# Kernel tuning notes

Measured on AMD Instinct MI355X. Metric: run time of the kernel, lower is better.

## Reference

```python
import jax, jax.numpy as jnp
import numpy as np

N = 50000      # nodes
E = 800000     # edges (before self-loops)
B = 50         # graphs in batch
F_IN = 16      # node features
HID = 64       # hidden_dim (= per-head channels, concat=False)
H = 4          # heads
ED = 5         # edge_dim
OUT = 3        # output_dim


def setup_inputs() -> dict:
    key = jax.random.key(0)
    ks = jax.random.split(key, 32)
    g = lambda k, shape, s=0.1: jax.random.normal(k, shape, dtype=jnp.float32) * s
    x = jax.random.normal(ks[0], (N, F_IN), dtype=jnp.float32)
    edge_index = jax.random.randint(ks[1], (2, E), 0, N)
    edge_attr = jax.random.normal(ks[2], (E, ED), dtype=jnp.float32)
    batch = jnp.repeat(jnp.arange(B), N // B)  # sorted segment ids, each graph non-empty
    inp = dict(
        x=x, edge_index=edge_index, edge_attr=edge_attr, batch=batch,
        # edge_encoder: Linear(5,64) -> ReLU -> Linear(64,1) -> Sigmoid
        ee_w1=g(ks[3], (ED, HID)), ee_b1=jnp.zeros((HID,), jnp.float32),
        ee_w2=g(ks[4], (HID, 1)), ee_b2=jnp.zeros((1,), jnp.float32),
        # GATConv params (PyG, edge_dim=1 semantics for the scalar edge weight)
        W1=g(ks[5], (F_IN, H * HID)),              # conv1 lin (bias=False)
        Ws=g(ks[6], (2, HID, H * HID)),            # convs[0..1] lin
        att_src=g(ks[7], (3, H, HID)),
        att_dst=g(ks[8], (3, H, HID)),
        We=g(ks[9], (3, 1, H * HID)),              # lin_edge (bias=False)
        att_e=g(ks[10], (3, H, HID)),
        bias=jnp.zeros((3, HID), jnp.float32),     # conv bias (concat=False -> [HID])
        ln_g=jnp.ones((HID,), jnp.float32), ln_b=jnp.zeros((HID,), jnp.float32),
        lin1_w=g(ks[11], (HID, HID)), lin1_b=jnp.zeros((HID,), jnp.float32),
        lin2_w=g(ks[12], (HID, OUT)), lin2_b=jnp.zeros((OUT,), jnp.float32),
    )
    return inp


def _gat_conv(xin, src, dst, ew, W, a_s, a_d, W_e, a_e, b):
    # xin: [N, Fin]; src/dst: [Et]; ew: [Et] per-edge scalar weight
    h = (xin @ W).reshape(N, H, HID)                      # [N,H,C]
    alpha_src = (h * a_s).sum(-1)                         # [N,H]
    alpha_dst = (h * a_d).sum(-1)                         # [N,H]
    he = (ew[:, None] * W_e.reshape(1, H * HID)).reshape(-1, H, HID)  # lin_edge
    alpha_e = (he * a_e).sum(-1)                          # [Et,H]
    alpha = jax.nn.leaky_relu(alpha_src[src] + alpha_dst[dst] + alpha_e, 0.2)
    # segment softmax over destination nodes
    m = jax.ops.segment_max(alpha, dst, num_segments=N)   # [N,H]
    p = jnp.exp(alpha - m[dst])
    s = jax.ops.segment_sum(p, dst, num_segments=N)
    a = p / (s[dst] + 1e-16)                              # [Et,H]
    out = jax.ops.segment_sum(h[src] * a[:, :, None], dst, num_segments=N)  # [N,H,C]
    return out.mean(axis=1) + b                           # concat=False -> mean heads


def reference(x, edge_index, edge_attr, batch, ee_w1, ee_b1, ee_w2, ee_b2,
              W1, Ws, att_src, att_dst, We, att_e, bias,
              ln_g, ln_b, lin1_w, lin1_b, lin2_w, lin2_b):
    # edge-attribute MLP -> per-edge scalar weight in (0,1)
    ew = jax.nn.sigmoid(jax.nn.relu(edge_attr @ ee_w1 + ee_b1) @ ee_w2 + ee_b2).reshape(-1)
    # add self-loops (PyG default, fill_value='mean' for edge weight)
    loops = jnp.arange(N)
    src = jnp.concatenate([edge_index[0], loops])
    dst = jnp.concatenate([edge_index[1], loops])
    ew = jnp.concatenate([ew, jnp.full((N,), ew.mean(), dtype=ew.dtype)])

    xi = jax.nn.elu(_gat_conv(x, src, dst, ew, W1, att_src[0], att_dst[0], We[0], att_e[0], bias[0]))
    for l in range(2):  # residual layers (dropout is identity in eval)
        xn = _gat_conv(xi, src, dst, ew, Ws[l], att_src[l + 1], att_dst[l + 1], We[l + 1], att_e[l + 1], bias[l + 1])
        xi = jax.nn.elu(xi + xn)

    mu = xi.mean(-1, keepdims=True)
    var = ((xi - mu) ** 2).mean(-1, keepdims=True)
    xln = (xi - mu) / jnp.sqrt(var + 1e-5) * ln_g + ln_b

    targets = jnp.searchsorted(batch, jnp.arange(B))      # first node of each graph
    t = jax.nn.elu(xln[targets] @ lin1_w + lin1_b)
    return t @ lin2_w + lin2_b                            # [B, 3]
```

## Files before the change

kernel.cpp:

```cpp
#include <hip/hip_runtime.h>
#include <cstddef>
#include <cstdint>

constexpr int NN = 50000;
constexpr int NE = 800000;
constexpr int ET = NE + NN;
constexpr int NB = 50;
constexpr int SCAN_B = 1024;
constexpr int NBLK = (NN + SCAN_B - 1) / SCAN_B;
constexpr int NPB_F = 16;
constexpr int NPB_T = 8;
constexpr int NTB_F = NN / NPB_F;
constexpr int MLPB = (ET + 1023) / 1024;

typedef float v2f __attribute__((ext_vector_type(2)));

__device__ __forceinline__ float eluf(float x) { return x > 0.f ? x : expm1f(x); }

__device__ __forceinline__ unsigned short f2bf(float f) {
    unsigned int u = __float_as_uint(f);
    unsigned int r = (u + 0x7fffu + ((u >> 16) & 1u)) >> 16;
    return (unsigned short)r;
}

template <int NPB, typename NodeOf>
__device__ __forceinline__ void alpha_reduce_store(const float* acc, float as_t, float ad_t,
                                                   int lane, int head, NodeOf nodeOf,
                                                   float* __restrict__ asrc,
                                                   float* __restrict__ adst) {
    #pragma unroll
    for (int g = 0; g < NPB; g += 4) {
        float x0, x1, x2, x3;
        {
            float vs, vd;
            vs = acc[g + 0] * as_t; vd = acc[g + 0] * ad_t;
            x0 = ((lane & 1) ? vd : vs) + __shfl_xor((lane & 1) ? vs : vd, 1);
            vs = acc[g + 1] * as_t; vd = acc[g + 1] * ad_t;
            x1 = ((lane & 1) ? vd : vs) + __shfl_xor((lane & 1) ? vs : vd, 1);
            vs = acc[g + 2] * as_t; vd = acc[g + 2] * ad_t;
            x2 = ((lane & 1) ? vd : vs) + __shfl_xor((lane & 1) ? vs : vd, 1);
            vs = acc[g + 3] * as_t; vd = acc[g + 3] * ad_t;
            x3 = ((lane & 1) ? vd : vs) + __shfl_xor((lane & 1) ? vs : vd, 1);
        }
        float y0 = ((lane & 2) ? x1 : x0) + __shfl_xor((lane & 2) ? x0 : x1, 2);
        float y1 = ((lane & 2) ? x3 : x2) + __shfl_xor((lane & 2) ? x2 : x3, 2);
        float z  = ((lane & 4) ? y1 : y0) + __shfl_xor((lane & 4) ? y0 : y1, 4);
        z += __shfl_xor(z, 8);
        z += __shfl_xor(z, 16);
        z += __shfl_xor(z, 32);
        if (lane < 8) {
            int node = nodeOf(g + (lane >> 1));
            if (lane & 1) adst[node * 4 + head] = z;
            else          asrc[node * 4 + head] = z;
        }
    }
}

__device__ __forceinline__ void aggregate_one_node(
        int widx, int lane,
        const unsigned short* __restrict__ hb,
        const float* __restrict__ asrc, const float* __restrict__ adst,
        const int2* __restrict__ csr, const float* __restrict__ ce_l,
        const float* __restrict__ bias_l, const int* __restrict__ row_ptr,
        float* __restrict__ xi, int residual) {
    int half = lane >> 5;
    int li = lane & 31;
    int head = li >> 3;
    int start = row_ptr[widx], end = row_ptr[widx + 1];
    float adw = adst[widx * 4 + head];
    float ceh = ce_l[head];
    const uint4* hbv = (const uint4*)hb;

    v2f acc2[4];
    #pragma unroll
    for (int r = 0; r < 4; ++r) { acc2[r].x = 0.f; acc2[r].y = 0.f; }
    float psum = 0.f;

    #define PROC(EI)                                                                  \
        {                                                                             \
            const int2 se = csr[EI];                                                  \
            int s = se.x;                                                             \
            float w = __int_as_float(se.y);                                           \
            const uint4 q = hbv[(unsigned)s * 32u + (unsigned)li];                    \
            float v = asrc[s * 4 + head] + adw + w * ceh;                             \
            v = v > 0.f ? v : 0.2f * v;                                               \
            float p = __expf(v);                                                      \
            psum += p;                                                                \
            v2f pv; pv.x = p; pv.y = p;                                               \
            v2f h0; h0.x = __uint_as_float(q.x << 16); h0.y = __uint_as_float(q.x & 0xffff0000u); \
            v2f h1; h1.x = __uint_as_float(q.y << 16); h1.y = __uint_as_float(q.y & 0xffff0000u); \
            v2f h2; h2.x = __uint_as_float(q.z << 16); h2.y = __uint_as_float(q.z & 0xffff0000u); \
            v2f h3; h3.x = __uint_as_float(q.w << 16); h3.y = __uint_as_float(q.w & 0xffff0000u); \
            acc2[0] += pv * h0;                                                       \
            acc2[1] += pv * h1;                                                       \
            acc2[2] += pv * h2;                                                       \
            acc2[3] += pv * h3;                                                       \
        }

    int ei = start + half;
    for (; ei + 2 < end; ei += 4) {
        PROC(ei);
        PROC(ei + 2);
    }
    if (ei < end) PROC(ei);
    #undef PROC

    float acc[8];
    acc[0] = acc2[0].x; acc[1] = acc2[0].y; acc[2] = acc2[1].x; acc[3] = acc2[1].y;
    acc[4] = acc2[2].x; acc[5] = acc2[2].y; acc[6] = acc2[3].x; acc[7] = acc2[3].y;

    psum += __shfl_xor(psum, 32);
    #pragma unroll
    for (int r = 0; r < 8; ++r) acc[r] += __shfl_xor(acc[r], 32);

    float inv = 1.f / (psum + 1e-16f);
    #pragma unroll
    for (int r = 0; r < 8; ++r) acc[r] *= inv;

    #pragma unroll
    for (int r = 0; r < 8; ++r) {
        acc[r] += __shfl_xor(acc[r], 8);
        acc[r] += __shfl_xor(acc[r], 16);
        acc[r] *= 0.25f;
    }

    if (lane < 8) {
        int c0 = lane * 8;
        const float4 b0 = *(const float4*)(bias_l + c0);
        const float4 b1 = *(const float4*)(bias_l + c0 + 4);
        float4 v0, v1;
        v0.x = acc[0] + b0.x; v0.y = acc[1] + b0.y; v0.z = acc[2] + b0.z; v0.w = acc[3] + b0.w;
        v1.x = acc[4] + b1.x; v1.y = acc[5] + b1.y; v1.z = acc[6] + b1.z; v1.w = acc[7] + b1.w;
        float* xo = xi + (size_t)widx * 64 + c0;
        if (residual) {
            const float4 p0 = *(const float4*)xo;
            const float4 p1 = *(const float4*)(xo + 4);
            v0.x += p0.x; v0.y += p0.y; v0.z += p0.z; v0.w += p0.w;
            v1.x += p1.x; v1.y += p1.y; v1.z += p1.z; v1.w += p1.w;
        }
        v0.x = eluf(v0.x); v0.y = eluf(v0.y); v0.z = eluf(v0.z); v0.w = eluf(v0.w);
        v1.x = eluf(v1.x); v1.y = eluf(v1.y); v1.z = eluf(v1.z); v1.w = eluf(v1.w);
        *(float4*)xo = v0;
        *(float4*)(xo + 4) = v1;
    }
}

__global__ void front_kernel(const float* __restrict__ xin, const float* __restrict__ W,
                             const float* __restrict__ a_s, const float* __restrict__ a_d,
                             unsigned short* __restrict__ hb, float* __restrict__ asrc,
                             float* __restrict__ adst,
                             const float* __restrict__ ea,
                             const float* __restrict__ w1, const float* __restrict__ b1,
                             const float* __restrict__ w2, const float* __restrict__ b2,
                             const int* __restrict__ ei_dst, int* __restrict__ deg,
                             int2* __restrict__ ewp, float* __restrict__ ew_sum) {
    __shared__ float wt[64 * 8];
    __shared__ float wsum[4];
    __shared__ unsigned short hs[NPB_F * 256];
    const int t = threadIdx.x;
    if (blockIdx.x < NTB_F) {
        const int FIN = 16;
        const int n0 = blockIdx.x * NPB_F;
        float acc[NPB_F];
        #pragma unroll
        for (int i = 0; i < NPB_F; ++i) acc[i] = 0.f;
        #pragma unroll 4
        for (int k = 0; k < FIN; ++k) {
            float wv = W[k * 256 + t];
            #pragma unroll
            for (int i = 0; i < NPB_F; ++i)
                acc[i] += xin[(size_t)(n0 + i) * FIN + k] * wv;
        }
        int lane = t & 63, head = t >> 6;
        #pragma unroll
        for (int i = 0; i < NPB_F; ++i) hs[i * 256 + t] = f2bf(acc[i]);
        alpha_reduce_store<NPB_F>(acc, a_s[t], a_d[t], lane, head,
                                  [&](int i) { return n0 + i; }, asrc, adst);
        __syncthreads();
        ((uint4*)(hb + (size_t)n0 * 256))[t]       = ((const uint4*)hs)[t];
        ((uint4*)(hb + (size_t)n0 * 256))[t + 256] = ((const uint4*)hs)[t + 256];
    } else {
        if (t < 64) {
            #pragma unroll
            for (int i = 0; i < 5; ++i) wt[t * 8 + i] = w1[i * 64 + t];
            wt[t * 8 + 5] = b1[t];
            wt[t * 8 + 6] = w2[t];
            wt[t * 8 + 7] = 0.f;
        }
        __syncthreads();
        const int e0 = (blockIdx.x - NTB_F) * 1024 + t;
        float a0[4], a1[4], a2[4], a3[4], a4[4], acc[4];
        #pragma unroll
        for (int m = 0; m < 4; ++m) {
            int e = e0 + 256 * m;
            if (e < NE) {
                a0[m] = ea[e*5+0]; a1[m] = ea[e*5+1]; a2[m] = ea[e*5+2];
                a3[m] = ea[e*5+3]; a4[m] = ea[e*5+4];
            } else {
                a0[m] = a1[m] = a2[m] = a3[m] = a4[m] = 0.f;
            }
            acc[m] = b2[0];
        }
        int pos[4] = {0, 0, 0, 0};
        #pragma unroll
        for (int m = 0; m < 4; ++m) {
            int e = e0 + 256 * m;
            if (e < ET) {
                int d = (e < NE) ? ei_dst[e] : (e - NE);
                pos[m] = atomicAdd(&deg[d], 1);
            }
        }
        #pragma unroll 4
        for (int j = 0; j < 64; ++j) {
            const float4 lo = *(const float4*)&wt[j * 8];
            const float4 hi = *(const float4*)&wt[j * 8 + 4];
            #pragma unroll
            for (int m = 0; m < 4; ++m) {
                float hj = hi.y + a0[m]*lo.x + a1[m]*lo.y + a2[m]*lo.z + a3[m]*lo.w + a4[m]*hi.x;
                acc[m] += fmaxf(hj, 0.f) * hi.z;
            }
        }
        float vsum = 0.f;
        #pragma unroll
        for (int m = 0; m < 4; ++m) {
            int e = e0 + 256 * m;
            if (e < NE) {
                float val = 1.f / (1.f + __expf(-acc[m]));
                ewp[e] = make_int2(pos[m], __float_as_int(val));
                vsum += val;
            } else if (e < ET) {
                ewp[e] = make_int2(pos[m], 0);
            }
        }
        #pragma unroll
        for (int m = 1; m <= 32; m <<= 1) vsum += __shfl_xor(vsum, m);
        if ((t & 63) == 0) wsum[t >> 6] = vsum;
        __syncthreads();
        if (t == 0) atomicAdd(ew_sum, (wsum[0] + wsum[1]) + (wsum[2] + wsum[3]));
    }
}

__global__ void scan_blocks(const int* __restrict__ deg, int* __restrict__ row_ptr,
                            int* __restrict__ bsum,
                            const float* __restrict__ We, const float* __restrict__ att_e,
                            float* __restrict__ ce) {
    __shared__ int sdata[SCAN_B];
    int t = threadIdx.x;
    int i = blockIdx.x * SCAN_B + t;
    if (i < 12) {
        int l = i >> 2, h = i & 3;
        float s = 0.f;
        for (int c = 0; c < 64; ++c)
            s += We[l*256 + h*64 + c] * att_e[l*256 + h*64 + c];
        ce[i] = s;
    }
    int v = (i < NN) ? deg[i] : 0;
    sdata[t] = v;
    __syncthreads();
    for (int off = 1; off < SCAN_B; off <<= 1) {
        int tv = (t >= off) ? sdata[t - off] : 0;
        __syncthreads();
        sdata[t] += tv;
        __syncthreads();
    }
    if (i < NN) row_ptr[i + 1] = sdata[t];
    if (t == SCAN_B - 1) bsum[blockIdx.x] = sdata[t];
}

__global__ void scan_fixup(const int* __restrict__ bsum, int* __restrict__ row_ptr) {
    __shared__ int sboff[64];
    int t = threadIdx.x;
    if (t < 64) {
        int v = (t < NBLK) ? bsum[t] : 0;
        int inc = v;
        #pragma unroll
        for (int off = 1; off < 64; off <<= 1) {
            int n = __shfl_up(inc, off);
            if (t >= off) inc += n;
        }
        sboff[t] = inc - v;
    }
    __syncthreads();
    int i = blockIdx.x * 256 + t;
    if (i < NN) row_ptr[i + 1] += sboff[i >> 10];
    if (i == 0) row_ptr[0] = 0;
}

__global__ void scatter_kernel(const int* __restrict__ ei_src, const int* __restrict__ ei_dst,
                               const int* __restrict__ row_ptr, const int2* __restrict__ ewp,
                               const float* __restrict__ ew_sum, int2* __restrict__ csr) {
    int e = blockIdx.x * 256 + threadIdx.x;
    if (e >= ET) return;
    int2 pw = ewp[e];
    int d, s, wbits;
    if (e < NE) {
        d = ei_dst[e];
        s = ei_src[e];
        wbits = pw.y;
    } else {
        d = s = e - NE;
        wbits = __float_as_int(ew_sum[0] * (1.f / (float)NE));
    }
    csr[row_ptr[d] + pw.x] = make_int2(s, wbits);
}

__global__ void mark1_kernel(const int* __restrict__ batch, const int* __restrict__ row_ptr,
                             const int2* __restrict__ csr, int* __restrict__ flag1,
                             int* __restrict__ list1, int* __restrict__ cnt1,
                             int* __restrict__ tgt) {
    int b = blockIdx.x;
    int t = threadIdx.x;
    __shared__ int tg_s;
    if (t == 0) {
        int lo = 0, hi = NN;
        while (lo < hi) {
            int mid = (lo + hi) >> 1;
            if (batch[mid] < b) lo = mid + 1; else hi = mid;
        }
        tg_s = lo;
        tgt[b] = lo;
    }
    __syncthreads();
    int tg = tg_s;
    int start = row_ptr[tg], end = row_ptr[tg + 1];
    for (int j = start + t; j < end; j += 64) {
        int s = csr[j].x;
        if (atomicExch(&flag1[s], 1) == 0) {
            int p = atomicAdd(cnt1, 1);
            if (p < NN) list1[p] = s;
        }
    }
}

__global__ void mark2_kernel(const int* __restrict__ row_ptr, const int2* __restrict__ csr,
                             const int* __restrict__ list1, const int* __restrict__ cnt1,
                             int* __restrict__ flag2, int* __restrict__ list2,
                             int* __restrict__ cnt2) {
    int i = blockIdx.x * 256 + threadIdx.x;
    if (i >= cnt1[0] || i >= NN) return;
    int u = list1[i];
    int start = row_ptr[u], end = row_ptr[u + 1];
    for (int j = start; j < end; ++j) {
        int s = csr[j].x;
        if (atomicExch(&flag2[s], 1) == 0) {
            int p = atomicAdd(cnt2, 1);
            if (p < NN) list2[p] = s;
        }
    }
}

__global__ void transform64_list(const int* __restrict__ list, const int* __restrict__ cnt,
                                 const float* __restrict__ xin, const float* __restrict__ W,
                                 const float* __restrict__ a_s, const float* __restrict__ a_d,
                                 unsigned short* __restrict__ hb, float* __restrict__ asrc,
                                 float* __restrict__ adst) {
    const int t = threadIdx.x;
    const int n0 = blockIdx.x * NPB_T;
    const int nv = min(cnt[0], NN);
    if (n0 >= nv) return;
    __shared__ unsigned short hs[NPB_T * 256];
    __shared__ int nls[NPB_T];
    if (t < NPB_T) nls[t] = list[min(n0 + t, nv - 1)];
    __syncthreads();
    int nreg[NPB_T];
    #pragma unroll
    for (int i = 0; i < NPB_T; ++i) nreg[i] = nls[i];
    float acc[NPB_T];
    #pragma unroll
    for (int i = 0; i < NPB_T; ++i) acc[i] = 0.f;
    #pragma unroll 4
    for (int k = 0; k < 64; ++k) {
        float wv = W[k * 256 + t];
        #pragma unroll
        for (int i = 0; i < NPB_T; ++i)
            acc[i] += xin[(size_t)nreg[i] * 64 + k] * wv;
    }
    int lane = t & 63, head = t >> 6;
    #pragma unroll
    for (int i = 0; i < NPB_T; ++i) hs[i * 256 + t] = f2bf(acc[i]);
    alpha_reduce_store<NPB_T>(acc, a_s[t], a_d[t], lane, head,
                              [&](int i) { return nls[i]; }, asrc, adst);
    __syncthreads();
    int nn = nls[t >> 5];
    ((uint4*)(hb + (size_t)nn * 256))[t & 31] = ((const uint4*)hs)[t];
}

__global__ void gat_aggregate_list(const int* __restrict__ list, const int* __restrict__ cnt,
                                   int cnt_const,
                                   const unsigned short* __restrict__ hb,
                                   const float* __restrict__ asrc, const float* __restrict__ adst,
                                   const int2* __restrict__ csr, const float* __restrict__ ce_l,
                                   const float* __restrict__ bias_l,
                                   const int* __restrict__ row_ptr,
                                   float* __restrict__ xi, int residual) {
    int idx = (blockIdx.x * 256 + threadIdx.x) >> 6;
    int n = cnt ? min(cnt[0], NN) : cnt_const;
    if (idx >= n) return;
    int widx = list[idx];
    int lane = threadIdx.x & 63;
    aggregate_one_node(widx, lane, hb, asrc, adst, csr, ce_l, bias_l, row_ptr, xi, residual);
}

__global__ void readout_kernel(const float* __restrict__ xi, const int* __restrict__ tgt,
                               const float* __restrict__ ln_g, const float* __restrict__ ln_b,
                               const float* __restrict__ l1w, const float* __restrict__ l1b,
                               const float* __restrict__ l2w, const float* __restrict__ l2b,
                               float* __restrict__ out) {
    int b = blockIdx.x;
    int t = threadIdx.x;
    int tg = tgt[b];
    float x = xi[(size_t)tg * 64 + t];
    float s = x;
    #pragma unroll
    for (int mask = 1; mask <= 32; mask <<= 1) s += __shfl_xor(s, mask);
    float mu = s * (1.f / 64.f);
    float d = x - mu;
    float v = d * d;
    #pragma unroll
    for (int mask = 1; mask <= 32; mask <<= 1) v += __shfl_xor(v, mask);
    float var = v * (1.f / 64.f);
    float xn = d * rsqrtf(var + 1e-5f) * ln_g[t] + ln_b[t];
    __shared__ float sx[64];
    sx[t] = xn;
    __syncthreads();
    float acc = l1b[t];
    for (int k = 0; k < 64; ++k) acc += sx[k] * l1w[k * 64 + t];
    acc = eluf(acc);
    __shared__ float st[64];
    st[t] = acc;
    __syncthreads();
    if (t < 3) {
        float o = l2b[t];
        for (int k = 0; k < 64; ++k) o += st[k] * l2w[k * 3 + t];
        out[b * 3 + t] = o;
    }
}

extern "C" void kernel_launch(void* const* d_in, const int* in_sizes, int n_in,
                              void* d_out, int out_size, void* d_ws, size_t ws_size,
                              hipStream_t stream) {
    const float* x        = (const float*)d_in[0];
    const int*   ei       = (const int*)d_in[1];
    const float* ea       = (const float*)d_in[2];
    const int*   batch    = (const int*)d_in[3];
    const float* ee_w1    = (const float*)d_in[4];
    const float* ee_b1    = (const float*)d_in[5];
    const float* ee_w2    = (const float*)d_in[6];
    const float* ee_b2    = (const float*)d_in[7];
    const float* W1       = (const float*)d_in[8];
    const float* Ws       = (const float*)d_in[9];
    const float* att_src  = (const float*)d_in[10];
    const float* att_dst  = (const float*)d_in[11];
    const float* We       = (const float*)d_in[12];
    const float* att_e    = (const float*)d_in[13];
    const float* bias     = (const float*)d_in[14];
    const float* ln_g     = (const float*)d_in[15];
    const float* ln_b     = (const float*)d_in[16];
    const float* lin1_w   = (const float*)d_in[17];
    const float* lin1_b   = (const float*)d_in[18];
    const float* lin2_w   = (const float*)d_in[19];
    const float* lin2_b   = (const float*)d_in[20];
    float* out = (float*)d_out;

    char* ws = (char*)d_ws;
    size_t off = 0;
    auto alloc = [&](size_t bytes) -> char* {
        char* p = ws + off;
        off += (bytes + 255) & ~(size_t)255;
        return p;
    };
    int2*  ewp     = (int2*)alloc((size_t)ET * 8);
    float* ce      = (float*)alloc(12 * 4);
    unsigned short* hbuf = (unsigned short*)alloc((size_t)NN * 256 * 2);
    float* asrc    = (float*)alloc((size_t)NN * 4 * 4);
    float* adst    = (float*)alloc((size_t)NN * 4 * 4);
    float* xi      = (float*)alloc((size_t)NN * 64 * 4);
    int*   deg     = (int*)alloc(((size_t)NN * 3 + 64) * 4);
    int*   flag1   = deg + NN;
    int*   flag2   = deg + 2 * NN;
    float* ew_sum  = (float*)(deg + 3 * NN);
    int*   cnt1    = deg + 3 * NN + 1;
    int*   cnt2    = deg + 3 * NN + 2;
    int*   row_ptr = (int*)alloc((size_t)(NN + 1) * 4);
    int*   bsum    = (int*)alloc(64 * 4);
    int2*  csr     = (int2*)alloc((size_t)ET * 8);
    int*   list1   = (int*)alloc((size_t)NN * 4);
    int*   list2   = (int*)alloc((size_t)NN * 4);
    int*   tgt     = (int*)alloc(NB * 4);
    (void)ws_size; (void)n_in; (void)in_sizes; (void)out_size;

    const int* ei_src = ei;
    const int* ei_dst = ei + NE;

    hipMemsetAsync(deg, 0, ((size_t)NN * 3 + 64) * 4, stream);
    front_kernel<<<NTB_F + MLPB, 256, 0, stream>>>(x, W1, att_src + 0 * 256, att_dst + 0 * 256,
                                                   hbuf, asrc, adst,
                                                   ea, ee_w1, ee_b1, ee_w2, ee_b2,
                                                   ei_dst, deg, ewp, ew_sum);

    scan_blocks<<<NBLK, SCAN_B, 0, stream>>>(deg, row_ptr, bsum, We, att_e, ce);
    scan_fixup<<<(NN + 255) / 256, 256, 0, stream>>>(bsum, row_ptr);
    scatter_kernel<<<(ET + 255) / 256, 256, 0, stream>>>(ei_src, ei_dst, row_ptr, ewp, ew_sum, csr);

    mark1_kernel<<<NB, 64, 0, stream>>>(batch, row_ptr, csr, flag1, list1, cnt1, tgt);
    mark2_kernel<<<(NN + 255) / 256, 256, 0, stream>>>(row_ptr, csr, list1, cnt1,
                                                       flag2, list2, cnt2);

    gat_aggregate_list<<<(NN + 3) / 4, 256, 0, stream>>>(list2, cnt2, 0, hbuf, asrc, adst,
                                                         csr, ce + 0 * 4, bias + 0 * 64,
                                                         row_ptr, xi, 0);
    transform64_list<<<NN / NPB_T, 256, 0, stream>>>(list2, cnt2, xi, Ws + 0 * 64 * 256,
                                                     att_src + 1 * 256, att_dst + 1 * 256,
                                                     hbuf, asrc, adst);
    gat_aggregate_list<<<(NN + 3) / 4, 256, 0, stream>>>(list1, cnt1, 0, hbuf, asrc, adst,
                                                         csr, ce + 1 * 4, bias + 1 * 64,
                                                         row_ptr, xi, 1);
    transform64_list<<<NN / NPB_T, 256, 0, stream>>>(list1, cnt1, xi, Ws + 1 * 64 * 256,
                                                     att_src + 2 * 256, att_dst + 2 * 256,
                                                     hbuf, asrc, adst);
    gat_aggregate_list<<<(NB + 3) / 4, 256, 0, stream>>>(tgt, nullptr, NB, hbuf, asrc, adst,
                                                         csr, ce + 2 * 4, bias + 2 * 64,
                                                         row_ptr, xi, 1);

    readout_kernel<<<NB, 64, 0, stream>>>(xi, tgt, ln_g, ln_b, lin1_w, lin1_b, lin2_w, lin2_b, out);
}
```

Measured before the change: 301.6 us.

## Mark receptive-field nodes from raw edges and scatter only needed CSR rows

Computes the 1-hop and 2-hop target neighbourhood flags directly from the raw edge list, folded into the front and scan kernels as extra blocks, instead of separate mark kernels that walk the CSR. The scatter kernel then writes CSR entries only for destinations in the 2-hop set, which cuts scatter writes. The last-layer aggregation is fused with the readout, removing two launches. The cost is extra full edge passes with atomics inside front and scan, and the ordering now relies on flag1 being complete before the scan kernel's marking blocks run.

```diff
diff --git a/kernel.cpp b/kernel.cpp
--- a/kernel.cpp
+++ b/kernel.cpp
@@ -12,6 +12,8 @@
 constexpr int NPB_T = 8;
 constexpr int NTB_F = NN / NPB_F;
 constexpr int MLPB = (ET + 1023) / 1024;
+constexpr int MRKB  = (ET + 255) / 256;
+constexpr int MRK2B = (ET + 1023) / 1024;
 
 typedef float v2f __attribute__((ext_vector_type(2)));
 
@@ -56,13 +58,14 @@
     }
 }
 
+template <bool WRITE_LDS>
 __device__ __forceinline__ void aggregate_one_node(
         int widx, int lane,
         const unsigned short* __restrict__ hb,
         const float* __restrict__ asrc, const float* __restrict__ adst,
         const int2* __restrict__ csr, const float* __restrict__ ce_l,
         const float* __restrict__ bias_l, const int* __restrict__ row_ptr,
-        float* __restrict__ xi, int residual) {
+        float* __restrict__ xi, int residual, float* xs_row) {
     int half = lane >> 5;
     int li = lane & 31;
     int head = li >> 3;
@@ -142,6 +145,10 @@
         v1.x = eluf(v1.x); v1.y = eluf(v1.y); v1.z = eluf(v1.z); v1.w = eluf(v1.w);
         *(float4*)xo = v0;
         *(float4*)(xo + 4) = v1;
+        if (WRITE_LDS) {
+            *(float4*)(xs_row + c0) = v0;
+            *(float4*)(xs_row + c0 + 4) = v1;
+        }
     }
 }
 
@@ -152,8 +159,11 @@
                              const float* __restrict__ ea,
                              const float* __restrict__ w1, const float* __restrict__ b1,
                              const float* __restrict__ w2, const float* __restrict__ b2,
-                             const int* __restrict__ ei_dst, int* __restrict__ deg,
-                             int2* __restrict__ ewp, float* __restrict__ ew_sum) {
+                             const int* __restrict__ ei_src, const int* __restrict__ ei_dst,
+                             int* __restrict__ deg,
+                             int2* __restrict__ ewp, float* __restrict__ ew_sum,
+                             const int* __restrict__ batch, int* __restrict__ flag1,
+                             int* __restrict__ list1, int* __restrict__ cnt1) {
     __shared__ float wt[64 * 8];
     __shared__ float wsum[4];
     __shared__ unsigned short hs[NPB_F * 256];
@@ -179,7 +189,7 @@
         __syncthreads();
         ((uint4*)(hb + (size_t)n0 * 256))[t]       = ((const uint4*)hs)[t];
         ((uint4*)(hb + (size_t)n0 * 256))[t + 256] = ((const uint4*)hs)[t + 256];
-    } else {
+    } else if (blockIdx.x < NTB_F + MLPB) {
         if (t < 64) {
             #pragma unroll
             for (int i = 0; i < 5; ++i) wt[t * 8 + i] = w1[i * 64 + t];
@@ -237,15 +247,41 @@
         if ((t & 63) == 0) wsum[t >> 6] = vsum;
         __syncthreads();
         if (t == 0) atomicAdd(ew_sum, (wsum[0] + wsum[1]) + (wsum[2] + wsum[3]));
+    } else {
+        int e = (blockIdx.x - NTB_F - MLPB) * 256 + t;
+        if (e < ET) {
+            int d, s;
+            if (e < NE) { d = ei_dst[e]; s = ei_src[e]; } else { d = s = e - NE; }
+            bool is_t = (d == 0) || (batch[d] != batch[d - 1]);
+            if (is_t && atomicExch(&flag1[s], 1) == 0) {
+                int p = atomicAdd(cnt1, 1);
+                if (p < NN) list1[p] = s;
+            }
+        }
     }
 }
 
 __global__ void scan_blocks(const int* __restrict__ deg, int* __restrict__ row_ptr,
                             int* __restrict__ bsum,
                             const float* __restrict__ We, const float* __restrict__ att_e,
-                            float* __restrict__ ce) {
+                            float* __restrict__ ce,
+                            const int* __restrict__ ei_src, const int* __restrict__ ei_dst,
+                            const int* __restrict__ flag1, int* __restrict__ flag2,
+                            int* __restrict__ list2, int* __restrict__ cnt2) {
     __shared__ int sdata[SCAN_B];
     int t = threadIdx.x;
+    if (blockIdx.x >= NBLK) {
+        int e = (blockIdx.x - NBLK) * 1024 + t;
+        if (e < ET) {
+            int d, s;
+            if (e < NE) { d = ei_dst[e]; s = ei_src[e]; } else { d = s = e - NE; }
+            if (flag1[d] && atomicExch(&flag2[s], 1) == 0) {
+                int p = atomicAdd(cnt2, 1);
+                if (p < NN) list2[p] = s;
+            }
+        }
+        return;
+    }
     int i = blockIdx.x * SCAN_B + t;
     if (i < 12) {
         int l = i >> 2, h = i & 3;
@@ -288,65 +324,22 @@
 
 __global__ void scatter_kernel(const int* __restrict__ ei_src, const int* __restrict__ ei_dst,
                                const int* __restrict__ row_ptr, const int2* __restrict__ ewp,
-                               const float* __restrict__ ew_sum, int2* __restrict__ csr) {
+                               const float* __restrict__ ew_sum, const int* __restrict__ flag2,
+                               int2* __restrict__ csr) {
     int e = blockIdx.x * 256 + threadIdx.x;
     if (e >= ET) return;
+    int d = (e < NE) ? ei_dst[e] : (e - NE);
+    if (!flag2[d]) return;
     int2 pw = ewp[e];
-    int d, s, wbits;
+    int s, wbits;
     if (e < NE) {
-        d = ei_dst[e];
         s = ei_src[e];
         wbits = pw.y;
     } else {
-        d = s = e - NE;
+        s = d;
         wbits = __float_as_int(ew_sum[0] * (1.f / (float)NE));
     }
     csr[row_ptr[d] + pw.x] = make_int2(s, wbits);
-}
-
-__global__ void mark1_kernel(const int* __restrict__ batch, const int* __restrict__ row_ptr,
-                             const int2* __restrict__ csr, int* __restrict__ flag1,
-                             int* __restrict__ list1, int* __restrict__ cnt1,
-                             int* __restrict__ tgt) {
-    int b = blockIdx.x;
-    int t = threadIdx.x;
-    __shared__ int tg_s;
-    if (t == 0) {
-        int lo = 0, hi = NN;
-        while (lo < hi) {
-            int mid = (lo + hi) >> 1;
-            if (batch[mid] < b) lo = mid + 1; else hi = mid;
-        }
-        tg_s = lo;
-        tgt[b] = lo;
-    }
-    __syncthreads();
-    int tg = tg_s;
-    int start = row_ptr[tg], end = row_ptr[tg + 1];
-    for (int j = start + t; j < end; j += 64) {
-        int s = csr[j].x;
-        if (atomicExch(&flag1[s], 1) == 0) {
-            int p = atomicAdd(cnt1, 1);
-            if (p < NN) list1[p] = s;
-        }
-    }
-}
-
-__global__ void mark2_kernel(const int* __restrict__ row_ptr, const int2* __restrict__ csr,
-                             const int* __restrict__ list1, const int* __restrict__ cnt1,
-                             int* __restrict__ flag2, int* __restrict__ list2,
-                             int* __restrict__ cnt2) {
-    int i = blockIdx.x * 256 + threadIdx.x;
-    if (i >= cnt1[0] || i >= NN) return;
-    int u = list1[i];
-    int start = row_ptr[u], end = row_ptr[u + 1];
-    for (int j = start; j < end; ++j) {
-        int s = csr[j].x;
-        if (atomicExch(&flag2[s], 1) == 0) {
-            int p = atomicAdd(cnt2, 1);
-            if (p < NN) list2[p] = s;
-        }
-    }
 }
 
 __global__ void transform64_list(const int* __restrict__ list, const int* __restrict__ cnt,
@@ -386,7 +379,6 @@
 }
 
 __global__ void gat_aggregate_list(const int* __restrict__ list, const int* __restrict__ cnt,
-                                   int cnt_const,
                                    const unsigned short* __restrict__ hb,
                                    const float* __restrict__ asrc, const float* __restrict__ adst,
                                    const int2* __restrict__ csr, const float* __restrict__ ce_l,
@@ -394,22 +386,41 @@
                                    const int* __restrict__ row_ptr,
                                    float* __restrict__ xi, int residual) {
     int idx = (blockIdx.x * 256 + threadIdx.x) >> 6;
-    int n = cnt ? min(cnt[0], NN) : cnt_const;
+    int n = min(cnt[0], NN);
     if (idx >= n) return;
     int widx = list[idx];
     int lane = threadIdx.x & 63;
-    aggregate_one_node(widx, lane, hb, asrc, adst, csr, ce_l, bias_l, row_ptr, xi, residual);
-}
-
-__global__ void readout_kernel(const float* __restrict__ xi, const int* __restrict__ tgt,
-                               const float* __restrict__ ln_g, const float* __restrict__ ln_b,
-                               const float* __restrict__ l1w, const float* __restrict__ l1b,
-                               const float* __restrict__ l2w, const float* __restrict__ l2b,
-                               float* __restrict__ out) {
+    aggregate_one_node<false>(widx, lane, hb, asrc, adst, csr, ce_l, bias_l, row_ptr,
+                              xi, residual, nullptr);
+}
+
+__global__ void readout_fused(const int* __restrict__ batch,
+                              const unsigned short* __restrict__ hb,
+                              const float* __restrict__ asrc, const float* __restrict__ adst,
+                              const int2* __restrict__ csr, const float* __restrict__ ce_l,
+                              const float* __restrict__ bias_l, const int* __restrict__ row_ptr,
+                              float* __restrict__ xi,
+                              const float* __restrict__ ln_g, const float* __restrict__ ln_b,
+                              const float* __restrict__ l1w, const float* __restrict__ l1b,
+                              const float* __restrict__ l2w, const float* __restrict__ l2b,
+                              float* __restrict__ out) {
     int b = blockIdx.x;
     int t = threadIdx.x;
-    int tg = tgt[b];
-    float x = xi[(size_t)tg * 64 + t];
+    __shared__ int tg_s;
+    __shared__ float xs[64];
+    if (t == 0) {
+        int lo = 0, hi = NN;
+        while (lo < hi) {
+            int mid = (lo + hi) >> 1;
+            if (batch[mid] < b) lo = mid + 1; else hi = mid;
+        }
+        tg_s = lo;
+    }
+    __syncthreads();
+    int tg = tg_s;
+    aggregate_one_node<true>(tg, t, hb, asrc, adst, csr, ce_l, bias_l, row_ptr, xi, 1, xs);
+    __syncthreads();
+    float x = xs[t];
     float s = x;
     #pragma unroll
     for (int mask = 1; mask <= 32; mask <<= 1) s += __shfl_xor(s, mask);
@@ -420,11 +431,11 @@
     for (int mask = 1; mask <= 32; mask <<= 1) v += __shfl_xor(v, mask);
     float var = v * (1.f / 64.f);
     float xn = d * rsqrtf(var + 1e-5f) * ln_g[t] + ln_b[t];
-    __shared__ float sx[64];
-    sx[t] = xn;
+    __syncthreads();
+    xs[t] = xn;
     __syncthreads();
     float acc = l1b[t];
-    for (int k = 0; k < 64; ++k) acc += sx[k] * l1w[k * 64 + t];
+    for (int k = 0; k < 64; ++k) acc += xs[k] * l1w[k * 64 + t];
     acc = eluf(acc);
     __shared__ float st[64];
     st[t] = acc;
@@ -486,41 +497,37 @@
     int2*  csr     = (int2*)alloc((size_t)ET * 8);
     int*   list1   = (int*)alloc((size_t)NN * 4);
     int*   list2   = (int*)alloc((size_t)NN * 4);
-    int*   tgt     = (int*)alloc(NB * 4);
     (void)ws_size; (void)n_in; (void)in_sizes; (void)out_size;
 
     const int* ei_src = ei;
     const int* ei_dst = ei + NE;
 
     hipMemsetAsync(deg, 0, ((size_t)NN * 3 + 64) * 4, stream);
-    front_kernel<<<NTB_F + MLPB, 256, 0, stream>>>(x, W1, att_src + 0 * 256, att_dst + 0 * 256,
-                                                   hbuf, asrc, adst,
-                                                   ea, ee_w1, ee_b1, ee_w2, ee_b2,
-                                                   ei_dst, deg, ewp, ew_sum);
-
-    scan_blocks<<<NBLK, SCAN_B, 0, stream>>>(deg, row_ptr, bsum, We, att_e, ce);
+    front_kernel<<<NTB_F + MLPB + MRKB, 256, 0, stream>>>(
+        x, W1, att_src + 0 * 256, att_dst + 0 * 256, hbuf, asrc, adst,
+        ea, ee_w1, ee_b1, ee_w2, ee_b2, ei_src, ei_dst, deg, ewp, ew_sum,
+        batch, flag1, list1, cnt1);
+
+    scan_blocks<<<NBLK + MRK2B, SCAN_B, 0, stream>>>(deg, row_ptr, bsum, We, att_e, ce,
+                                                     ei_src, ei_dst, flag1, flag2, list2, cnt2);
     scan_fixup<<<(NN + 255) / 256, 256, 0, stream>>>(bsum, row_ptr);
-    scatter_kernel<<<(ET + 255) / 256, 256, 0, stream>>>(ei_src, ei_dst, row_ptr, ewp, ew_sum, csr);
-
-    mark1_kernel<<<NB, 64, 0, stream>>>(batch, row_ptr, csr, flag1, list1, cnt1, tgt);
-    mark2_kernel<<<(NN + 255) / 256, 256, 0, stream>>>(row_ptr, csr, list1, cnt1,
-                                                       flag2, list2, cnt2);
-
-    gat_aggregate_list<<<(NN + 3) / 4, 256, 0, stream>>>(list2, cnt2, 0, hbuf, asrc, adst,
+    scatter_kernel<<<(ET + 255) / 256, 256, 0, stream>>>(ei_src, ei_dst, row_ptr, ewp,
+                                                         ew_sum, flag2, csr);
+
+    gat_aggregate_list<<<(NN + 3) / 4, 256, 0, stream>>>(list2, cnt2, hbuf, asrc, adst,
                                                          csr, ce + 0 * 4, bias + 0 * 64,
                                                          row_ptr, xi, 0);
     transform64_list<<<NN / NPB_T, 256, 0, stream>>>(list2, cnt2, xi, Ws + 0 * 64 * 256,
                                                      att_src + 1 * 256, att_dst + 1 * 256,
                                                      hbuf, asrc, adst);
-    gat_aggregate_list<<<(NN + 3) / 4, 256, 0, stream>>>(list1, cnt1, 0, hbuf, asrc, adst,
+    gat_aggregate_list<<<(NN + 3) / 4, 256, 0, stream>>>(list1, cnt1, hbuf, asrc, adst,
                                                          csr, ce + 1 * 4, bias + 1 * 64,
                                                          row_ptr, xi, 1);
     transform64_list<<<NN / NPB_T, 256, 0, stream>>>(list1, cnt1, xi, Ws + 1 * 64 * 256,
                                                      att_src + 2 * 256, att_dst + 2 * 256,
                                                      hbuf, asrc, adst);
-    gat_aggregate_list<<<(NB + 3) / 4, 256, 0, stream>>>(tgt, nullptr, NB, hbuf, asrc, adst,
-                                                         csr, ce + 2 * 4, bias + 2 * 64,
-                                                         row_ptr, xi, 1);
-
-    readout_kernel<<<NB, 64, 0, stream>>>(xi, tgt, ln_g, ln_b, lin1_w, lin1_b, lin2_w, lin2_b, out);
-}
+
+    readout_fused<<<NB, 64, 0, stream>>>(batch, hbuf, asrc, adst, csr, ce + 2 * 4,
+                                         bias + 2 * 64, row_ptr, xi,
+                                         ln_g, ln_b, lin1_w, lin1_b, lin2_w, lin2_b, out);
+}
```

After: 338.1 us. +12.1%, slower.
